# Kernel optimization log

Hardware: AMD Instinct MI355X
Metric: run time of the kernel (lower is better)

The kernel has to match this reference:

```python
import jax, jax.numpy as jnp
import numpy as np

B, S, IN, HID, OUT = 8, 4096, 128, 128, 1

def setup_inputs() -> dict:
    key = jax.random.key(0)
    ks = jax.random.split(key, 16)
    xav = lambda k, i, o: jax.random.normal(k, (i, o), jnp.float32) * np.sqrt(2.0 / (i + o))
    return {
        'x': jax.random.normal(ks[0], (B, S, IN), jnp.float32),
        'm1': xav(ks[1], IN, HID), 'b1': jnp.zeros((1, 1, HID), jnp.float32),
        'm2': xav(ks[2], HID, HID), 'b2': jnp.zeros((1, 1, HID), jnp.float32),
        'wq': xav(ks[3], HID, HID), 'wk': xav(ks[4], HID, HID), 'wv': xav(ks[5], HID, HID),
        'ml0': xav(ks[6], 128, 64), 'bl0': jnp.zeros((1, 1, 64), jnp.float32),
        'ml1': xav(ks[7], 64, 32), 'bl1': jnp.zeros((1, 1, 32), jnp.float32),
        'm3': xav(ks[8], 32, OUT), 'b3': jnp.zeros((1, 1, OUT), jnp.float32),
        'atten_size': 5,
    }

def reference(x, m1, b1, m2, b2, wq, wk, wv, ml0, bl0, ml1, bl1, m3, b3, atten_size):
    a = atten_size
    h = jax.nn.relu(x @ m1 + b1)
    h = jax.nn.relu(h @ m2 + b2)            # [B,S,H]
    vals = h @ wv
    pad_cfg = ((0, 0), (a, a), (0, 0))
    padded = jnp.pad(h, pad_cfg)
    padded_v = jnp.pad(vals, pad_cfg)
    # window gather via roll, matching torch.roll(padded, k, 1) for k=-a..a, then slice
    x_nei = jnp.stack([jnp.roll(padded, k, axis=1) for k in range(-a, a + 1)], axis=2)[:, a:-a]   # [B,S,W,H]
    v_nei = jnp.stack([jnp.roll(padded_v, k, axis=1) for k in range(-a, a + 1)], axis=2)[:, a:-a]
    keys = x_nei @ wk                        # [B,S,W,H]
    query = h @ wq                           # [B,S,H]
    scale = 1.0 / np.sqrt(float(HID))
    dot = jnp.einsum('bswh,bsh->bsw', keys, query) * scale
    atten_w = jax.nn.softmax(dot, axis=2)    # [B,S,W]
    o = jnp.einsum('bsw,bswh->bsh', atten_w, v_nei)
    o = jax.nn.relu(o @ ml0 + bl0)
    o = jax.nn.relu(o @ ml1 + bl1)
    o = jax.nn.sigmoid(o @ m3 + b3)          # [B,S,OUT]
    return (o, atten_w)
```

## Files before the change

### kernel.cpp

```cpp
#include <hip/hip_runtime.h>
#include <hip/hip_bf16.h>
#include <math.h>

#define SEQ 4096
#define NB 8
#define CHUNK 64
#define HALO 5
#define WIN 11
#define MROWS 80
#define AROWS 74
#define HSTR 136
#define NT 512
#define CNT 256

typedef short s16x8 __attribute__((ext_vector_type(8)));
typedef float f32x4 __attribute__((ext_vector_type(4)));

__device__ __forceinline__ unsigned short f2bf(float f) {
    return __builtin_bit_cast(unsigned short, __float2bfloat16(f));
}

#define OFF_M1  0
#define OFF_M2  16384
#define OFF_WQK 32768
#define OFF_WV  49152
#define OFF_ML0 65536
#define OFF_ML1 73728
#define CONV_A  59392
#define WS_ELEMS 75776

__global__ void convert_weights(const float* __restrict__ m1, const float* __restrict__ m2,
                                const float* __restrict__ wq, const float* __restrict__ wk,
                                const float* __restrict__ wv, const float* __restrict__ ml0,
                                const float* __restrict__ ml1, unsigned short* __restrict__ ws)
{
    int idx = blockIdx.x * CNT + threadIdx.x;
    if (idx < 16384) {
        ws[OFF_M1 + idx] = f2bf(m1[(idx & 127) * 128 + (idx >> 7)]);
    } else if (idx < 32768) {
        int r = idx - 16384;
        ws[OFF_M2 + r] = f2bf(m2[(r & 127) * 128 + (r >> 7)]);
    } else if (idx < 49152) {
        int r = idx - 32768;
        ws[OFF_WV + r] = f2bf(wv[(r & 127) * 128 + (r >> 7)]);
    } else if (idx < 57344) {
        int r = idx - 49152;
        ws[OFF_ML0 + r] = f2bf(ml0[(r & 127) * 64 + (r >> 7)]);
    } else if (idx < CONV_A) {
        int r = idx - 57344;
        ws[OFF_ML1 + r] = f2bf(ml1[(r & 63) * 32 + (r >> 6)]);
    } else if (idx < WS_ELEMS) {
        int r = idx - CONV_A;
        int d = r >> 7, e = r & 127;
        const float4* qa = (const float4*)(wq + e * 128);
        const float4* ka = (const float4*)(wk + d * 128);
        float a0 = 0.f, a1 = 0.f, a2 = 0.f, a3 = 0.f;
        #pragma unroll
        for (int c = 0; c < 32; ++c) {
            float4 A = qa[c], B = ka[c];
            a0 = fmaf(A.x, B.x, a0); a1 = fmaf(A.y, B.y, a1);
            a2 = fmaf(A.z, B.z, a2); a3 = fmaf(A.w, B.w, a3);
        }
        ws[OFF_WQK + r] = f2bf((a0 + a1 + a2 + a3) * 0.08838834764831845f);
    }
}

__device__ __forceinline__ void loadB4(s16x8 d[4], const unsigned short* __restrict__ wt,
                                       int ct, int l15, int hi)
{
    const unsigned short* p = wt + (ct * 16 + l15) * 128 + hi * 8;
    d[0] = *(const s16x8*)(p);
    d[1] = *(const s16x8*)(p + 32);
    d[2] = *(const s16x8*)(p + 64);
    d[3] = *(const s16x8*)(p + 96);
}

template<int MT, bool RELU, bool BIAS>
__device__ __forceinline__ void gemmS(const unsigned short* __restrict__ src,
                                      const s16x8 bf[4],
                                      const float* __restrict__ bias,
                                      unsigned short* __restrict__ dst,
                                      int l15, int hi, int wave)
{
    f32x4 acc[MT];
    #pragma unroll
    for (int i = 0; i < MT; ++i) acc[i] = (f32x4){0.f, 0.f, 0.f, 0.f};
    const unsigned short* arow = src + l15 * HSTR + hi * 8;
    #pragma unroll
    for (int ks = 0; ks < 4; ++ks)
        #pragma unroll
        for (int rt = 0; rt < MT; ++rt) {
            s16x8 a = *(const s16x8*)(arow + rt * 16 * HSTR + ks * 32);
            acc[rt] = __builtin_amdgcn_mfma_f32_16x16x32_bf16(a, bf[ks], acc[rt], 0, 0, 0);
        }
    const int c = wave * 16 + l15;
    const float bb = BIAS ? bias[c] : 0.f;
    #pragma unroll
    for (int rt = 0; rt < MT; ++rt)
        #pragma unroll
        for (int j = 0; j < 4; ++j) {
            float v = acc[rt][j] + bb;
            if (RELU) v = fmaxf(v, 0.f);
            dst[(rt * 16 + hi * 4 + j) * HSTR + c] = f2bf(v);
        }
}

__global__ __launch_bounds__(NT, 4)
void ExLRestSelfAtten_mfma(const float* __restrict__ x,
                           const float* __restrict__ b1, const float* __restrict__ b2,
                           const float* __restrict__ bl0, const float* __restrict__ bl1,
                           const float* __restrict__ m3, const float* __restrict__ b3,
                           const unsigned short* __restrict__ wsw,
                           float* __restrict__ out0, float* __restrict__ attw)
{
    __shared__ __align__(16) unsigned short bufA[MROWS * HSTR];
    __shared__ __align__(16) unsigned short bufB[MROWS * HSTR];
    __shared__ __align__(16) unsigned short qbuf[CHUNK * HSTR];
    __shared__ __align__(16) float sbuf[4 * 16 * 36];
    __shared__ __align__(16) float saw [CHUNK * WIN];

    unsigned short* h64 = bufA;
    float* fbuf = (float*)(bufA + 4608);

    const int t = threadIdx.x;
    const int lane = t & 63, wave = t >> 6;
    const int l15 = lane & 15, hi = lane >> 4;
    const int bx = blockIdx.x;
    const int b = bx >> 6;
    const int cstart = (bx & 63) * CHUNK;

    s16x8 wA[4], wB[4], wml0[4], wml1[2];
    loadB4(wA, wsw + OFF_M1, wave, l15, hi);

    const float* xb = x + (size_t)b * SEQ * 128;
    for (int idx = t; idx < MROWS * 32; idx += NT) {
        int r = idx >> 5, k4 = (idx & 31) << 2;
        int p = cstart - HALO + r;
        float4 v = make_float4(0.f, 0.f, 0.f, 0.f);
        if (r < AROWS && p >= 0 && p < SEQ) v = *(const float4*)(xb + (size_t)p * 128 + k4);
        ushort4 o;
        o.x = f2bf(v.x); o.y = f2bf(v.y); o.z = f2bf(v.z); o.w = f2bf(v.w);
        *(ushort4*)(bufA + r * HSTR + k4) = o;
    }
    __syncthreads();

    loadB4(wB, wsw + OFF_M2, wave, l15, hi);
    gemmS<5, true, true>(bufA, wA, b1, bufB, l15, hi, wave);
    __syncthreads();

    loadB4(wA, wsw + OFF_WQK, wave, l15, hi);
    gemmS<5, true, true>(bufB, wB, b2, bufA, l15, hi, wave);
    __syncthreads();

    loadB4(wB, wsw + OFF_WV, wave, l15, hi);
    gemmS<4, false, false>(bufA + HALO * HSTR, wA, nullptr, qbuf, l15, hi, wave);
    loadB4(wml0, wsw + OFF_ML0, wave & 3, l15, hi);
    gemmS<5, false, false>(bufA, wB, nullptr, bufB, l15, hi, wave);
    __syncthreads();

    {
        const unsigned short* p1 = wsw + OFF_ML1 + ((wave & 1) * 16 + l15) * 64 + hi * 8;
        wml1[0] = *(const s16x8*)(p1);
        wml1[1] = *(const s16x8*)(p1 + 32);
    }
    {
        const int rt = wave >> 1, kk = wave & 1, kt = rt + kk;
        f32x4 sacc = (f32x4){0.f, 0.f, 0.f, 0.f};
        #pragma unroll
        for (int ks = 0; ks < 4; ++ks) {
            s16x8 a  = *(const s16x8*)(qbuf + (rt * 16 + l15) * HSTR + ks * 32 + hi * 8);
            s16x8 hb = *(const s16x8*)(bufA + (kt * 16 + l15) * HSTR + ks * 32 + hi * 8);
            sacc = __builtin_amdgcn_mfma_f32_16x16x32_bf16(a, hb, sacc, 0, 0, 0);
        }
        #pragma unroll
        for (int j = 0; j < 4; ++j)
            sbuf[rt * 576 + (hi * 4 + j) * 36 + kk * 16 + l15] = sacc[j];
    }
    __syncthreads();

    if (t < CHUNK) {
        const int base = (t >> 4) * 576 + (t & 15) * 36 + (t & 15) + 10;
        float d[WIN], mx = -1e30f;
        #pragma unroll
        for (int w = 0; w < WIN; ++w) { d[w] = sbuf[base - w]; mx = fmaxf(mx, d[w]); }
        float sum = 0.f;
        #pragma unroll
        for (int w = 0; w < WIN; ++w) { d[w] = __expf(d[w] - mx); sum += d[w]; }
        float inv = 1.f / sum;
        #pragma unroll
        for (int w = 0; w < WIN; ++w) saw[t * WIN + w] = d[w] * inv;
    }
    __syncthreads();

    for (int idx = t; idx < CHUNK * 16; idx += NT) {
        int s = idx >> 4, c0 = (idx & 15) << 3;
        float acc[8] = {0.f, 0.f, 0.f, 0.f, 0.f, 0.f, 0.f, 0.f};
        #pragma unroll
        for (int w = 0; w < WIN; ++w) {
            float aw = saw[s * WIN + w];
            uint4 u = *(const uint4*)(bufB + (s + 10 - w) * HSTR + c0);
            unsigned uu[4] = {u.x, u.y, u.z, u.w};
            #pragma unroll
            for (int q = 0; q < 4; ++q) {
                acc[2 * q]     = fmaf(aw, __builtin_bit_cast(float, uu[q] << 16), acc[2 * q]);
                acc[2 * q + 1] = fmaf(aw, __builtin_bit_cast(float, uu[q] & 0xffff0000u), acc[2 * q + 1]);
            }
        }
        unsigned p0 = f2bf(acc[0]) | ((unsigned)f2bf(acc[1]) << 16);
        unsigned p1 = f2bf(acc[2]) | ((unsigned)f2bf(acc[3]) << 16);
        unsigned p2 = f2bf(acc[4]) | ((unsigned)f2bf(acc[5]) << 16);
        unsigned p3 = f2bf(acc[6]) | ((unsigned)f2bf(acc[7]) << 16);
        *(uint4*)(qbuf + s * HSTR + c0) = make_uint4(p0, p1, p2, p3);
    }
    {
        float* ab = attw + (size_t)(b * SEQ + cstart) * WIN;
        for (int idx = t; idx < CHUNK * WIN; idx += NT) ab[idx] = saw[idx];
    }
    __syncthreads();

    {
        const int ct4 = wave & 3;
        f32x4 acc[2] = {(f32x4){0.f,0.f,0.f,0.f}, (f32x4){0.f,0.f,0.f,0.f}};
        #pragma unroll
        for (int ks = 0; ks < 4; ++ks)
            #pragma unroll
            for (int q = 0; q < 2; ++q) {
                int rr = (wave >> 2) + 2 * q;
                s16x8 a = *(const s16x8*)(qbuf + (rr * 16 + l15) * HSTR + ks * 32 + hi * 8);
                acc[q] = __builtin_amdgcn_mfma_f32_16x16x32_bf16(a, wml0[ks], acc[q], 0, 0, 0);
            }
        int c = ct4 * 16 + l15;
        float bb = bl0[c];
        #pragma unroll
        for (int q = 0; q < 2; ++q)
            #pragma unroll
            for (int j = 0; j < 4; ++j)
                h64[(((wave >> 2) + 2 * q) * 16 + hi * 4 + j) * 72 + c] = f2bf(fmaxf(acc[q][j] + bb, 0.f));
    }
    __syncthreads();

    {
        const int rt2 = wave >> 1, ct2 = wave & 1;
        f32x4 acc = (f32x4){0.f, 0.f, 0.f, 0.f};
        #pragma unroll
        for (int ks = 0; ks < 2; ++ks) {
            s16x8 a = *(const s16x8*)(h64 + (rt2 * 16 + l15) * 72 + ks * 32 + hi * 8);
            acc = __builtin_amdgcn_mfma_f32_16x16x32_bf16(a, wml1[ks], acc, 0, 0, 0);
        }
        int c = ct2 * 16 + l15;
        float bb = bl1[c];
        #pragma unroll
        for (int j = 0; j < 4; ++j)
            fbuf[(rt2 * 16 + hi * 4 + j) * 36 + c] = fmaxf(acc[j] + bb, 0.f);
    }
    __syncthreads();

    if (t < CHUNK) {
        float acc = b3[0];
        #pragma unroll
        for (int k = 0; k < 32; ++k) acc = fmaf(fbuf[t * 36 + k], m3[k], acc);
        out0[(size_t)b * SEQ + cstart + t] = 1.f / (1.f + __expf(-acc));
    }
}

extern "C" void kernel_launch(void* const* d_in, const int* in_sizes, int n_in,
                              void* d_out, int out_size, void* d_ws, size_t ws_size,
                              hipStream_t stream)
{
    const float* x   = (const float*)d_in[0];
    const float* m1  = (const float*)d_in[1];
    const float* b1  = (const float*)d_in[2];
    const float* m2  = (const float*)d_in[3];
    const float* b2  = (const float*)d_in[4];
    const float* wq  = (const float*)d_in[5];
    const float* wk  = (const float*)d_in[6];
    const float* wv  = (const float*)d_in[7];
    const float* ml0 = (const float*)d_in[8];
    const float* bl0 = (const float*)d_in[9];
    const float* ml1 = (const float*)d_in[10];
    const float* bl1 = (const float*)d_in[11];
    const float* m3  = (const float*)d_in[12];
    const float* b3  = (const float*)d_in[13];

    float* out0 = (float*)d_out;
    float* attw = out0 + (size_t)NB * SEQ;

    unsigned short* wsw = (unsigned short*)d_ws;
    convert_weights<<<(WS_ELEMS + CNT - 1) / CNT, CNT, 0, stream>>>(
        m1, m2, wq, wk, wv, ml0, ml1, wsw);
    ExLRestSelfAtten_mfma<<<NB * (SEQ / CHUNK), NT, 0, stream>>>(
        x, b1, b2, bl0, bl1, m3, b3, wsw, out0, attw);
}
```

Baseline: 27.18 us.

## Fold Wv into ml0 and compute attention-weighted sum as banded MFMA GEMM

Precomputes Wv·ml0 as a single 128x64 weight so the value projection and first output layer collapse into one GEMM producing 64-wide values. The windowed weighted sum becomes an MFMA over a banded 64x96 probability matrix against the transposed projected values, replacing the scalar FMA loop. The MLP GEMMs are retiled so each wave computes a 48x32 tile over 96 padded rows, and Q and V projections run concurrently on separate wave halves. Shared memory is also trimmed by aliasing buffers. The cost is extra padded rows, a zero-filled probability buffer, and bf16 rounding of the probabilities and fused weights.

Measured after the change: 30.19 us. 11.0% more time.

```diff
diff --git a/kernel.cpp b/kernel.cpp
--- a/kernel.cpp
+++ b/kernel.cpp
@@ -7,9 +7,10 @@
 #define CHUNK 64
 #define HALO 5
 #define WIN 11
-#define MROWS 80
+#define MROWS 96
 #define AROWS 74
 #define HSTR 136
+#define PSTR 104
 #define NT 512
 #define CNT 256
 
@@ -23,11 +24,9 @@
 #define OFF_M1  0
 #define OFF_M2  16384
 #define OFF_WQK 32768
-#define OFF_WV  49152
-#define OFF_ML0 65536
-#define OFF_ML1 73728
-#define CONV_A  59392
-#define WS_ELEMS 75776
+#define OFF_WF  49152
+#define OFF_ML1 57344
+#define WS_ELEMS 59392
 
 __global__ void convert_weights(const float* __restrict__ m1, const float* __restrict__ m2,
                                 const float* __restrict__ wq, const float* __restrict__ wk,
@@ -36,21 +35,12 @@
 {
     int idx = blockIdx.x * CNT + threadIdx.x;
     if (idx < 16384) {
-        ws[OFF_M1 + idx] = f2bf(m1[(idx & 127) * 128 + (idx >> 7)]);
+        ws[idx] = f2bf(m1[(idx & 127) * 128 + (idx >> 7)]);
     } else if (idx < 32768) {
         int r = idx - 16384;
-        ws[OFF_M2 + r] = f2bf(m2[(r & 127) * 128 + (r >> 7)]);
+        ws[idx] = f2bf(m2[(r & 127) * 128 + (r >> 7)]);
     } else if (idx < 49152) {
         int r = idx - 32768;
-        ws[OFF_WV + r] = f2bf(wv[(r & 127) * 128 + (r >> 7)]);
-    } else if (idx < 57344) {
-        int r = idx - 49152;
-        ws[OFF_ML0 + r] = f2bf(ml0[(r & 127) * 64 + (r >> 7)]);
-    } else if (idx < CONV_A) {
-        int r = idx - 57344;
-        ws[OFF_ML1 + r] = f2bf(ml1[(r & 63) * 32 + (r >> 6)]);
-    } else if (idx < WS_ELEMS) {
-        int r = idx - CONV_A;
         int d = r >> 7, e = r & 127;
         const float4* qa = (const float4*)(wq + e * 128);
         const float4* ka = (const float4*)(wk + d * 128);
@@ -61,48 +51,68 @@
             a0 = fmaf(A.x, B.x, a0); a1 = fmaf(A.y, B.y, a1);
             a2 = fmaf(A.z, B.z, a2); a3 = fmaf(A.w, B.w, a3);
         }
-        ws[OFF_WQK + r] = f2bf((a0 + a1 + a2 + a3) * 0.08838834764831845f);
-    }
-}
-
-__device__ __forceinline__ void loadB4(s16x8 d[4], const unsigned short* __restrict__ wt,
-                                       int ct, int l15, int hi)
-{
-    const unsigned short* p = wt + (ct * 16 + l15) * 128 + hi * 8;
-    d[0] = *(const s16x8*)(p);
-    d[1] = *(const s16x8*)(p + 32);
-    d[2] = *(const s16x8*)(p + 64);
-    d[3] = *(const s16x8*)(p + 96);
-}
-
-template<int MT, bool RELU, bool BIAS>
-__device__ __forceinline__ void gemmS(const unsigned short* __restrict__ src,
-                                      const s16x8 bf[4],
-                                      const float* __restrict__ bias,
-                                      unsigned short* __restrict__ dst,
-                                      int l15, int hi, int wave)
-{
-    f32x4 acc[MT];
+        ws[idx] = f2bf((a0 + a1 + a2 + a3) * 0.08838834764831845f);
+    } else if (idx < 57344) {
+        int r = idx - 49152;
+        int n = r >> 7, k = r & 127;
+        const float* vr = wv + k * 128;
+        float a = 0.f;
+        #pragma unroll
+        for (int c = 0; c < 128; ++c) a = fmaf(vr[c], ml0[c * 64 + n], a);
+        ws[idx] = f2bf(a);
+    } else if (idx < WS_ELEMS) {
+        int r = idx - 57344;
+        int n = r >> 6, k = r & 63;
+        ws[idx] = f2bf(ml1[k * 32 + n]);
+    }
+}
+
+__device__ __forceinline__ void loadB24(s16x8 bf[2][4], const unsigned short* __restrict__ wt,
+                                        int cg, int l15, int hi)
+{
+    const unsigned short* wp = wt + (cg * 32 + l15) * 128 + hi * 8;
     #pragma unroll
-    for (int i = 0; i < MT; ++i) acc[i] = (f32x4){0.f, 0.f, 0.f, 0.f};
-    const unsigned short* arow = src + l15 * HSTR + hi * 8;
+    for (int ci = 0; ci < 2; ++ci)
+        #pragma unroll
+        for (int ks = 0; ks < 4; ++ks)
+            bf[ci][ks] = *(const s16x8*)(wp + ci * 16 * 128 + ks * 32);
+}
+
+template<bool RELU>
+__device__ __forceinline__ void gemm96(const unsigned short* __restrict__ src,
+                                       const s16x8 bf[2][4], const float* __restrict__ bias,
+                                       unsigned short* __restrict__ dst,
+                                       int l15, int hi, int rh, int cg)
+{
+    f32x4 acc[3][2];
+    #pragma unroll
+    for (int rt = 0; rt < 3; ++rt) {
+        acc[rt][0] = (f32x4){0.f, 0.f, 0.f, 0.f};
+        acc[rt][1] = (f32x4){0.f, 0.f, 0.f, 0.f};
+    }
+    const unsigned short* ap = src + (rh * 48 + l15) * HSTR + hi * 8;
     #pragma unroll
     for (int ks = 0; ks < 4; ++ks)
         #pragma unroll
-        for (int rt = 0; rt < MT; ++rt) {
-            s16x8 a = *(const s16x8*)(arow + rt * 16 * HSTR + ks * 32);
-            acc[rt] = __builtin_amdgcn_mfma_f32_16x16x32_bf16(a, bf[ks], acc[rt], 0, 0, 0);
-        }
-    const int c = wave * 16 + l15;
-    const float bb = BIAS ? bias[c] : 0.f;
+        for (int rt = 0; rt < 3; ++rt) {
+            s16x8 a = *(const s16x8*)(ap + rt * 16 * HSTR + ks * 32);
+            #pragma unroll
+            for (int ci = 0; ci < 2; ++ci)
+                acc[rt][ci] = __builtin_amdgcn_mfma_f32_16x16x32_bf16(a, bf[ci][ks], acc[rt][ci], 0, 0, 0);
+        }
     #pragma unroll
-    for (int rt = 0; rt < MT; ++rt)
-        #pragma unroll
-        for (int j = 0; j < 4; ++j) {
-            float v = acc[rt][j] + bb;
-            if (RELU) v = fmaxf(v, 0.f);
-            dst[(rt * 16 + hi * 4 + j) * HSTR + c] = f2bf(v);
-        }
+    for (int ci = 0; ci < 2; ++ci) {
+        const int c = cg * 32 + ci * 16 + l15;
+        const float bb = bias[c];
+        #pragma unroll
+        for (int rt = 0; rt < 3; ++rt)
+            #pragma unroll
+            for (int j = 0; j < 4; ++j) {
+                float v = acc[rt][ci][j] + bb;
+                if (RELU) v = fmaxf(v, 0.f);
+                dst[(rh * 48 + rt * 16 + hi * 4 + j) * HSTR + c] = f2bf(v);
+            }
+    }
 }
 
 __global__ __launch_bounds__(NT, 4)
@@ -116,11 +126,12 @@
     __shared__ __align__(16) unsigned short bufA[MROWS * HSTR];
     __shared__ __align__(16) unsigned short bufB[MROWS * HSTR];
     __shared__ __align__(16) unsigned short qbuf[CHUNK * HSTR];
-    __shared__ __align__(16) float sbuf[4 * 16 * 36];
-    __shared__ __align__(16) float saw [CHUNK * WIN];
-
-    unsigned short* h64 = bufA;
-    float* fbuf = (float*)(bufA + 4608);
+
+    unsigned short* vhb  = bufB;
+    float*          sbuf = (float*)(bufB + 6656);
+    unsigned short* pbuf = qbuf;
+    unsigned short* o2b  = bufA;
+    float*          fbuf = (float*)qbuf;
 
     const int t = threadIdx.x;
     const int lane = t & 63, wave = t >> 6;
@@ -128,9 +139,10 @@
     const int bx = blockIdx.x;
     const int b = bx >> 6;
     const int cstart = (bx & 63) * CHUNK;
-
-    s16x8 wA[4], wB[4], wml0[4], wml1[2];
-    loadB4(wA, wsw + OFF_M1, wave, l15, hi);
+    const int rh = wave >> 2, cg = wave & 3;
+
+    s16x8 wfr[2][4];
+    loadB24(wfr, wsw + OFF_M1, cg, l15, hi);
 
     const float* xb = x + (size_t)b * SEQ * 128;
     for (int idx = t; idx < MROWS * 32; idx += NT) {
@@ -144,37 +156,89 @@
     }
     __syncthreads();
 
-    loadB4(wB, wsw + OFF_M2, wave, l15, hi);
-    gemmS<5, true, true>(bufA, wA, b1, bufB, l15, hi, wave);
-    __syncthreads();
-
-    loadB4(wA, wsw + OFF_WQK, wave, l15, hi);
-    gemmS<5, true, true>(bufB, wB, b2, bufA, l15, hi, wave);
-    __syncthreads();
-
-    loadB4(wB, wsw + OFF_WV, wave, l15, hi);
-    gemmS<4, false, false>(bufA + HALO * HSTR, wA, nullptr, qbuf, l15, hi, wave);
-    loadB4(wml0, wsw + OFF_ML0, wave & 3, l15, hi);
-    gemmS<5, false, false>(bufA, wB, nullptr, bufB, l15, hi, wave);
+    gemm96<true>(bufA, wfr, b1, bufB, l15, hi, rh, cg);
+    loadB24(wfr, wsw + OFF_M2, cg, l15, hi);
+    __syncthreads();
+
+    gemm96<true>(bufB, wfr, b2, bufA, l15, hi, rh, cg);
+    __syncthreads();
+
+    if (wave < 4) {
+        const int qrh = wave >> 1, qcg = wave & 1;
+        f32x4 acc[2][4];
+        #pragma unroll
+        for (int rt = 0; rt < 2; ++rt)
+            #pragma unroll
+            for (int ct = 0; ct < 4; ++ct) acc[rt][ct] = (f32x4){0.f, 0.f, 0.f, 0.f};
+        const unsigned short* ap = bufA + (HALO + qrh * 32 + l15) * HSTR + hi * 8;
+        const unsigned short* wp = wsw + OFF_WQK + (qcg * 64 + l15) * 128 + hi * 8;
+        #pragma unroll
+        for (int ks = 0; ks < 4; ++ks) {
+            s16x8 a0 = *(const s16x8*)(ap + ks * 32);
+            s16x8 a1 = *(const s16x8*)(ap + 16 * HSTR + ks * 32);
+            #pragma unroll
+            for (int ct = 0; ct < 4; ++ct) {
+                s16x8 bb = *(const s16x8*)(wp + ct * 16 * 128 + ks * 32);
+                acc[0][ct] = __builtin_amdgcn_mfma_f32_16x16x32_bf16(a0, bb, acc[0][ct], 0, 0, 0);
+                acc[1][ct] = __builtin_amdgcn_mfma_f32_16x16x32_bf16(a1, bb, acc[1][ct], 0, 0, 0);
+            }
+        }
+        #pragma unroll
+        for (int rt = 0; rt < 2; ++rt)
+            #pragma unroll
+            for (int ct = 0; ct < 4; ++ct)
+                #pragma unroll
+                for (int j = 0; j < 4; ++j)
+                    qbuf[(qrh * 32 + rt * 16 + hi * 4 + j) * HSTR + qcg * 64 + ct * 16 + l15]
+                        = f2bf(acc[rt][ct][j]);
+    } else {
+        const int w4 = wave - 4;
+        const int vrh = w4 >> 1, vcg = w4 & 1;
+        f32x4 acc[3][2];
+        #pragma unroll
+        for (int rt = 0; rt < 3; ++rt) {
+            acc[rt][0] = (f32x4){0.f, 0.f, 0.f, 0.f};
+            acc[rt][1] = (f32x4){0.f, 0.f, 0.f, 0.f};
+        }
+        const unsigned short* ap = bufA + (vrh * 48 + l15) * HSTR + hi * 8;
+        const unsigned short* wp = wsw + OFF_WF + (vcg * 32 + l15) * 128 + hi * 8;
+        #pragma unroll
+        for (int ks = 0; ks < 4; ++ks) {
+            s16x8 b0 = *(const s16x8*)(wp + ks * 32);
+            s16x8 b1f = *(const s16x8*)(wp + 16 * 128 + ks * 32);
+            #pragma unroll
+            for (int rt = 0; rt < 3; ++rt) {
+                s16x8 a = *(const s16x8*)(ap + rt * 16 * HSTR + ks * 32);
+                acc[rt][0] = __builtin_amdgcn_mfma_f32_16x16x32_bf16(a, b0, acc[rt][0], 0, 0, 0);
+                acc[rt][1] = __builtin_amdgcn_mfma_f32_16x16x32_bf16(a, b1f, acc[rt][1], 0, 0, 0);
+            }
+        }
+        #pragma unroll
+        for (int ct = 0; ct < 2; ++ct) {
+            const int n = vcg * 32 + ct * 16 + l15;
+            #pragma unroll
+            for (int rt = 0; rt < 3; ++rt) {
+                ushort4 pk;
+                pk.x = f2bf(acc[rt][ct][0]); pk.y = f2bf(acc[rt][ct][1]);
+                pk.z = f2bf(acc[rt][ct][2]); pk.w = f2bf(acc[rt][ct][3]);
+                *(ushort4*)(vhb + n * PSTR + vrh * 48 + rt * 16 + hi * 4) = pk;
+            }
+        }
+    }
     __syncthreads();
 
     {
-        const unsigned short* p1 = wsw + OFF_ML1 + ((wave & 1) * 16 + l15) * 64 + hi * 8;
-        wml1[0] = *(const s16x8*)(p1);
-        wml1[1] = *(const s16x8*)(p1 + 32);
-    }
-    {
-        const int rt = wave >> 1, kk = wave & 1, kt = rt + kk;
+        const int srt = wave >> 1, kk = wave & 1, kt = srt + kk;
         f32x4 sacc = (f32x4){0.f, 0.f, 0.f, 0.f};
         #pragma unroll
         for (int ks = 0; ks < 4; ++ks) {
-            s16x8 a  = *(const s16x8*)(qbuf + (rt * 16 + l15) * HSTR + ks * 32 + hi * 8);
+            s16x8 a  = *(const s16x8*)(qbuf + (srt * 16 + l15) * HSTR + ks * 32 + hi * 8);
             s16x8 hb = *(const s16x8*)(bufA + (kt * 16 + l15) * HSTR + ks * 32 + hi * 8);
             sacc = __builtin_amdgcn_mfma_f32_16x16x32_bf16(a, hb, sacc, 0, 0, 0);
         }
         #pragma unroll
         for (int j = 0; j < 4; ++j)
-            sbuf[rt * 576 + (hi * 4 + j) * 36 + kk * 16 + l15] = sacc[j];
+            sbuf[srt * 576 + (hi * 4 + j) * 36 + kk * 16 + l15] = sacc[j];
     }
     __syncthreads();
 
@@ -187,78 +251,71 @@
         #pragma unroll
         for (int w = 0; w < WIN; ++w) { d[w] = __expf(d[w] - mx); sum += d[w]; }
         float inv = 1.f / sum;
-        #pragma unroll
-        for (int w = 0; w < WIN; ++w) saw[t * WIN + w] = d[w] * inv;
-    }
-    __syncthreads();
-
-    for (int idx = t; idx < CHUNK * 16; idx += NT) {
-        int s = idx >> 4, c0 = (idx & 15) << 3;
-        float acc[8] = {0.f, 0.f, 0.f, 0.f, 0.f, 0.f, 0.f, 0.f};
+        unsigned short* pr = pbuf + t * PSTR;
+        #pragma unroll
+        for (int i = 0; i < 12; ++i)
+            *(uint4*)(pr + i * 8) = make_uint4(0u, 0u, 0u, 0u);
+        float* ab = attw + (size_t)(b * SEQ + cstart + t) * WIN;
         #pragma unroll
         for (int w = 0; w < WIN; ++w) {
-            float aw = saw[s * WIN + w];
-            uint4 u = *(const uint4*)(bufB + (s + 10 - w) * HSTR + c0);
-            unsigned uu[4] = {u.x, u.y, u.z, u.w};
-            #pragma unroll
-            for (int q = 0; q < 4; ++q) {
-                acc[2 * q]     = fmaf(aw, __builtin_bit_cast(float, uu[q] << 16), acc[2 * q]);
-                acc[2 * q + 1] = fmaf(aw, __builtin_bit_cast(float, uu[q] & 0xffff0000u), acc[2 * q + 1]);
-            }
-        }
-        unsigned p0 = f2bf(acc[0]) | ((unsigned)f2bf(acc[1]) << 16);
-        unsigned p1 = f2bf(acc[2]) | ((unsigned)f2bf(acc[3]) << 16);
-        unsigned p2 = f2bf(acc[4]) | ((unsigned)f2bf(acc[5]) << 16);
-        unsigned p3 = f2bf(acc[6]) | ((unsigned)f2bf(acc[7]) << 16);
-        *(uint4*)(qbuf + s * HSTR + c0) = make_uint4(p0, p1, p2, p3);
-    }
+            float a = d[w] * inv;
+            ab[w] = a;
+            pr[t + 10 - w] = f2bf(a);
+        }
+    }
+    __syncthreads();
+
     {
-        float* ab = attw + (size_t)(b * SEQ + cstart) * WIN;
-        for (int idx = t; idx < CHUNK * WIN; idx += NT) ab[idx] = saw[idx];
+        const int ort = wave >> 1, ocp = wave & 1;
+        f32x4 acc[2] = {(f32x4){0.f,0.f,0.f,0.f}, (f32x4){0.f,0.f,0.f,0.f}};
+        #pragma unroll
+        for (int ks = 0; ks < 3; ++ks) {
+            s16x8 a = *(const s16x8*)(pbuf + (ort * 16 + l15) * PSTR + ks * 32 + hi * 8);
+            #pragma unroll
+            for (int ci = 0; ci < 2; ++ci) {
+                s16x8 bb = *(const s16x8*)(vhb + (ocp * 32 + ci * 16 + l15) * PSTR + ks * 32 + hi * 8);
+                acc[ci] = __builtin_amdgcn_mfma_f32_16x16x32_bf16(a, bb, acc[ci], 0, 0, 0);
+            }
+        }
+        #pragma unroll
+        for (int ci = 0; ci < 2; ++ci) {
+            const int c = ocp * 32 + ci * 16 + l15;
+            const float bb = bl0[c];
+            #pragma unroll
+            for (int j = 0; j < 4; ++j)
+                o2b[(ort * 16 + hi * 4 + j) * 72 + c] = f2bf(fmaxf(acc[ci][j] + bb, 0.f));
+        }
     }
     __syncthreads();
 
     {
-        const int ct4 = wave & 3;
-        f32x4 acc[2] = {(f32x4){0.f,0.f,0.f,0.f}, (f32x4){0.f,0.f,0.f,0.f}};
-        #pragma unroll
-        for (int ks = 0; ks < 4; ++ks)
-            #pragma unroll
-            for (int q = 0; q < 2; ++q) {
-                int rr = (wave >> 2) + 2 * q;
-                s16x8 a = *(const s16x8*)(qbuf + (rr * 16 + l15) * HSTR + ks * 32 + hi * 8);
-                acc[q] = __builtin_amdgcn_mfma_f32_16x16x32_bf16(a, wml0[ks], acc[q], 0, 0, 0);
-            }
-        int c = ct4 * 16 + l15;
-        float bb = bl0[c];
-        #pragma unroll
-        for (int q = 0; q < 2; ++q)
-            #pragma unroll
-            for (int j = 0; j < 4; ++j)
-                h64[(((wave >> 2) + 2 * q) * 16 + hi * 4 + j) * 72 + c] = f2bf(fmaxf(acc[q][j] + bb, 0.f));
-    }
-    __syncthreads();
-
-    {
-        const int rt2 = wave >> 1, ct2 = wave & 1;
+        const int hrt = wave >> 1, hct = wave & 1;
         f32x4 acc = (f32x4){0.f, 0.f, 0.f, 0.f};
+        const unsigned short* wp = wsw + OFF_ML1 + (hct * 16 + l15) * 64 + hi * 8;
         #pragma unroll
         for (int ks = 0; ks < 2; ++ks) {
-            s16x8 a = *(const s16x8*)(h64 + (rt2 * 16 + l15) * 72 + ks * 32 + hi * 8);
-            acc = __builtin_amdgcn_mfma_f32_16x16x32_bf16(a, wml1[ks], acc, 0, 0, 0);
-        }
-        int c = ct2 * 16 + l15;
-        float bb = bl1[c];
+            s16x8 a  = *(const s16x8*)(o2b + (hrt * 16 + l15) * 72 + ks * 32 + hi * 8);
+            s16x8 bb = *(const s16x8*)(wp + ks * 32);
+            acc = __builtin_amdgcn_mfma_f32_16x16x32_bf16(a, bb, acc, 0, 0, 0);
+        }
+        const int c = hct * 16 + l15;
+        const float bb = bl1[c];
         #pragma unroll
         for (int j = 0; j < 4; ++j)
-            fbuf[(rt2 * 16 + hi * 4 + j) * 36 + c] = fmaxf(acc[j] + bb, 0.f);
+            fbuf[(hrt * 16 + hi * 4 + j) * 36 + c] = fmaxf(acc[j] + bb, 0.f);
     }
     __syncthreads();
 
     if (t < CHUNK) {
         float acc = b3[0];
-        #pragma unroll
-        for (int k = 0; k < 32; ++k) acc = fmaf(fbuf[t * 36 + k], m3[k], acc);
+        const float* fr = fbuf + t * 36;
+        #pragma unroll
+        for (int k4 = 0; k4 < 8; ++k4) {
+            float4 hv = *(const float4*)(fr + k4 * 4);
+            float4 mv = *(const float4*)(m3 + k4 * 4);
+            acc = fmaf(hv.x, mv.x, acc); acc = fmaf(hv.y, mv.y, acc);
+            acc = fmaf(hv.z, mv.z, acc); acc = fmaf(hv.w, mv.w, acc);
+        }
         out0[(size_t)b * SEQ + cstart + t] = 1.f / (1.f + __expf(-acc));
     }
 }
```

## Fold value projection into first post-attention layer and fuse attention output stage

Applied to the files above, without the earlier changes.

Precomputes the product Wv·ml0 on the device during weight conversion, so the value GEMM produces 64 columns directly. The attention-weighted sum then applies bias and ReLU and feeds the ml1 layer, removing the separate 128-wide value GEMM over 80 rows, the ml0 GEMM and one barrier. The attention weights are also written to global memory straight from the softmax threads, and the final dot product is vectorised. Folding the two weights changes where bf16 rounding happens, and the combined weight is computed with a serial 128-term loop per element in the conversion kernel.

Result: faster. 25.23 us, median of 3 (-7.2%).

```diff
diff --git a/kernel.cpp b/kernel.cpp
--- a/kernel.cpp
+++ b/kernel.cpp
@@ -23,11 +23,9 @@
 #define OFF_M1  0
 #define OFF_M2  16384
 #define OFF_WQK 32768
-#define OFF_WV  49152
-#define OFF_ML0 65536
-#define OFF_ML1 73728
-#define CONV_A  59392
-#define WS_ELEMS 75776
+#define OFF_WF  49152
+#define OFF_ML1 57344
+#define WS_ELEMS 59392
 
 __global__ void convert_weights(const float* __restrict__ m1, const float* __restrict__ m2,
                                 const float* __restrict__ wq, const float* __restrict__ wk,
@@ -36,21 +34,12 @@
 {
     int idx = blockIdx.x * CNT + threadIdx.x;
     if (idx < 16384) {
-        ws[OFF_M1 + idx] = f2bf(m1[(idx & 127) * 128 + (idx >> 7)]);
+        ws[idx] = f2bf(m1[(idx & 127) * 128 + (idx >> 7)]);
     } else if (idx < 32768) {
         int r = idx - 16384;
-        ws[OFF_M2 + r] = f2bf(m2[(r & 127) * 128 + (r >> 7)]);
+        ws[idx] = f2bf(m2[(r & 127) * 128 + (r >> 7)]);
     } else if (idx < 49152) {
         int r = idx - 32768;
-        ws[OFF_WV + r] = f2bf(wv[(r & 127) * 128 + (r >> 7)]);
-    } else if (idx < 57344) {
-        int r = idx - 49152;
-        ws[OFF_ML0 + r] = f2bf(ml0[(r & 127) * 64 + (r >> 7)]);
-    } else if (idx < CONV_A) {
-        int r = idx - 57344;
-        ws[OFF_ML1 + r] = f2bf(ml1[(r & 63) * 32 + (r >> 6)]);
-    } else if (idx < WS_ELEMS) {
-        int r = idx - CONV_A;
         int d = r >> 7, e = r & 127;
         const float4* qa = (const float4*)(wq + e * 128);
         const float4* ka = (const float4*)(wk + d * 128);
@@ -61,7 +50,19 @@
             a0 = fmaf(A.x, B.x, a0); a1 = fmaf(A.y, B.y, a1);
             a2 = fmaf(A.z, B.z, a2); a3 = fmaf(A.w, B.w, a3);
         }
-        ws[OFF_WQK + r] = f2bf((a0 + a1 + a2 + a3) * 0.08838834764831845f);
+        ws[idx] = f2bf((a0 + a1 + a2 + a3) * 0.08838834764831845f);
+    } else if (idx < 57344) {
+        int r = idx - 49152;
+        int n = r >> 7, k = r & 127;
+        const float* vr = wv + k * 128;
+        float a = 0.f;
+        #pragma unroll
+        for (int c = 0; c < 128; ++c) a = fmaf(vr[c], ml0[c * 64 + n], a);
+        ws[idx] = f2bf(a);
+    } else if (idx < WS_ELEMS) {
+        int r = idx - 57344;
+        int n = r >> 6, k = r & 63;
+        ws[idx] = f2bf(ml1[k * 32 + n]);
     }
 }
 
@@ -119,8 +120,8 @@
     __shared__ __align__(16) float sbuf[4 * 16 * 36];
     __shared__ __align__(16) float saw [CHUNK * WIN];
 
-    unsigned short* h64 = bufA;
-    float* fbuf = (float*)(bufA + 4608);
+    unsigned short* o2b  = bufA;
+    float*          fbuf = (float*)qbuf;
 
     const int t = threadIdx.x;
     const int lane = t & 63, wave = t >> 6;
@@ -129,7 +130,7 @@
     const int b = bx >> 6;
     const int cstart = (bx & 63) * CHUNK;
 
-    s16x8 wA[4], wB[4], wml0[4], wml1[2];
+    s16x8 wA[4], wB[4], wml1[2];
     loadB4(wA, wsw + OFF_M1, wave, l15, hi);
 
     const float* xb = x + (size_t)b * SEQ * 128;
@@ -152,10 +153,27 @@
     gemmS<5, true, true>(bufB, wB, b2, bufA, l15, hi, wave);
     __syncthreads();
 
-    loadB4(wB, wsw + OFF_WV, wave, l15, hi);
+    loadB4(wB, wsw + OFF_WF, wave & 3, l15, hi);
     gemmS<4, false, false>(bufA + HALO * HSTR, wA, nullptr, qbuf, l15, hi, wave);
-    loadB4(wml0, wsw + OFF_ML0, wave & 3, l15, hi);
-    gemmS<5, false, false>(bufA, wB, nullptr, bufB, l15, hi, wave);
+    {
+        const int cg = wave & 3, rh = wave >> 2;
+        const int rt0 = rh ? 3 : 0, ntr = rh ? 2 : 3;
+        f32x4 acc[3];
+        #pragma unroll
+        for (int i = 0; i < 3; ++i) acc[i] = (f32x4){0.f, 0.f, 0.f, 0.f};
+        const unsigned short* arow = bufA + (rt0 * 16 + l15) * HSTR + hi * 8;
+        #pragma unroll
+        for (int ks = 0; ks < 4; ++ks)
+            for (int rt = 0; rt < ntr; ++rt) {
+                s16x8 a = *(const s16x8*)(arow + rt * 16 * HSTR + ks * 32);
+                acc[rt] = __builtin_amdgcn_mfma_f32_16x16x32_bf16(a, wB[ks], acc[rt], 0, 0, 0);
+            }
+        const int c = cg * 16 + l15;
+        for (int rt = 0; rt < ntr; ++rt)
+            #pragma unroll
+            for (int j = 0; j < 4; ++j)
+                bufB[((rt0 + rt) * 16 + hi * 4 + j) * HSTR + c] = f2bf(acc[rt][j]);
+    }
     __syncthreads();
 
     {
@@ -187,13 +205,18 @@
         #pragma unroll
         for (int w = 0; w < WIN; ++w) { d[w] = __expf(d[w] - mx); sum += d[w]; }
         float inv = 1.f / sum;
-        #pragma unroll
-        for (int w = 0; w < WIN; ++w) saw[t * WIN + w] = d[w] * inv;
-    }
-    __syncthreads();
-
-    for (int idx = t; idx < CHUNK * 16; idx += NT) {
-        int s = idx >> 4, c0 = (idx & 15) << 3;
+        float* ab = attw + (size_t)(b * SEQ + cstart + t) * WIN;
+        #pragma unroll
+        for (int w = 0; w < WIN; ++w) {
+            float a = d[w] * inv;
+            saw[t * WIN + w] = a;
+            ab[w] = a;
+        }
+    }
+    __syncthreads();
+
+    {
+        const int s = t >> 3, c0 = (t & 7) << 3;
         float acc[8] = {0.f, 0.f, 0.f, 0.f, 0.f, 0.f, 0.f, 0.f};
         #pragma unroll
         for (int w = 0; w < WIN; ++w) {
@@ -206,36 +229,14 @@
                 acc[2 * q + 1] = fmaf(aw, __builtin_bit_cast(float, uu[q] & 0xffff0000u), acc[2 * q + 1]);
             }
         }
-        unsigned p0 = f2bf(acc[0]) | ((unsigned)f2bf(acc[1]) << 16);
-        unsigned p1 = f2bf(acc[2]) | ((unsigned)f2bf(acc[3]) << 16);
-        unsigned p2 = f2bf(acc[4]) | ((unsigned)f2bf(acc[5]) << 16);
-        unsigned p3 = f2bf(acc[6]) | ((unsigned)f2bf(acc[7]) << 16);
-        *(uint4*)(qbuf + s * HSTR + c0) = make_uint4(p0, p1, p2, p3);
-    }
-    {
-        float* ab = attw + (size_t)(b * SEQ + cstart) * WIN;
-        for (int idx = t; idx < CHUNK * WIN; idx += NT) ab[idx] = saw[idx];
-    }
-    __syncthreads();
-
-    {
-        const int ct4 = wave & 3;
-        f32x4 acc[2] = {(f32x4){0.f,0.f,0.f,0.f}, (f32x4){0.f,0.f,0.f,0.f}};
-        #pragma unroll
-        for (int ks = 0; ks < 4; ++ks)
-            #pragma unroll
-            for (int q = 0; q < 2; ++q) {
-                int rr = (wave >> 2) + 2 * q;
-                s16x8 a = *(const s16x8*)(qbuf + (rr * 16 + l15) * HSTR + ks * 32 + hi * 8);
-                acc[q] = __builtin_amdgcn_mfma_f32_16x16x32_bf16(a, wml0[ks], acc[q], 0, 0, 0);
-            }
-        int c = ct4 * 16 + l15;
-        float bb = bl0[c];
-        #pragma unroll
-        for (int q = 0; q < 2; ++q)
-            #pragma unroll
-            for (int j = 0; j < 4; ++j)
-                h64[(((wave >> 2) + 2 * q) * 16 + hi * 4 + j) * 72 + c] = f2bf(fmaxf(acc[q][j] + bb, 0.f));
+        float4 bv0 = *(const float4*)(bl0 + c0);
+        float4 bv1 = *(const float4*)(bl0 + c0 + 4);
+        const float bb[8] = {bv0.x, bv0.y, bv0.z, bv0.w, bv1.x, bv1.y, bv1.z, bv1.w};
+        unsigned short pk[8];
+        #pragma unroll
+        for (int i = 0; i < 8; ++i) pk[i] = f2bf(fmaxf(acc[i] + bb[i], 0.f));
+        *(ushort4*)(o2b + s * 72 + c0) = *(ushort4*)(pk);
+        *(ushort4*)(o2b + s * 72 + c0 + 4) = *(ushort4*)(pk + 4);
     }
     __syncthreads();
 
@@ -244,11 +245,11 @@
         f32x4 acc = (f32x4){0.f, 0.f, 0.f, 0.f};
         #pragma unroll
         for (int ks = 0; ks < 2; ++ks) {
-            s16x8 a = *(const s16x8*)(h64 + (rt2 * 16 + l15) * 72 + ks * 32 + hi * 8);
+            s16x8 a = *(const s16x8*)(o2b + (rt2 * 16 + l15) * 72 + ks * 32 + hi * 8);
             acc = __builtin_amdgcn_mfma_f32_16x16x32_bf16(a, wml1[ks], acc, 0, 0, 0);
         }
-        int c = ct2 * 16 + l15;
-        float bb = bl1[c];
+        const int c = ct2 * 16 + l15;
+        const float bb = bl1[c];
         #pragma unroll
         for (int j = 0; j < 4; ++j)
             fbuf[(rt2 * 16 + hi * 4 + j) * 36 + c] = fmaxf(acc[j] + bb, 0.f);
@@ -257,8 +258,14 @@
 
     if (t < CHUNK) {
         float acc = b3[0];
-        #pragma unroll
-        for (int k = 0; k < 32; ++k) acc = fmaf(fbuf[t * 36 + k], m3[k], acc);
+        const float* fr = fbuf + t * 36;
+        #pragma unroll
+        for (int k4 = 0; k4 < 8; ++k4) {
+            float4 hv = *(const float4*)(fr + k4 * 4);
+            float4 mv = *(const float4*)(m3 + k4 * 4);
+            acc = fmaf(hv.x, mv.x, acc); acc = fmaf(hv.y, mv.y, acc);
+            acc = fmaf(hv.z, mv.z, acc); acc = fmaf(hv.w, mv.w, acc);
+        }
         out0[(size_t)b * SEQ + cstart + t] = 1.f / (1.f + __expf(-acc));
     }
 }
```
